# Performance work log

Measured on AMD Instinct MI355X. Metric: run time of the kernel, lower is better.

Reference implementation:

```python
import math
import jax, jax.numpy as jnp
import numpy as np

B, L, S, H, E, D = 2, 2048, 2048, 8, 64, 64


def setup_inputs() -> dict:
    key = jax.random.key(0)
    kq, kk, kv = jax.random.split(key, 3)
    return {
        "queries": jax.random.normal(kq, (B, L, H, E), dtype=jnp.float32),
        "keys": jax.random.normal(kk, (B, S, H, E), dtype=jnp.float32),
        "values": jax.random.normal(kv, (B, S, H, D), dtype=jnp.float32),
    }


def reference(queries, keys, values):
    b, l, h, e = queries.shape
    s = keys.shape[1]
    # source truncates queries if L > S
    if l > s:
        queries = queries[:, :s]
        l = s
    # dense scores [B,H,L,S]
    scores = jnp.einsum('blhe,bshe->bhls', queries, keys)
    # sparsity measure per query: max - mean over keys
    M_sp = scores.max(axis=-1) - scores.sum(axis=-1) / s  # [B,H,L]
    # k = min(max(L*log(S),1), L); for S>=3 this equals L (all queries, reordered)
    k = min(int(max(l * math.log(s), 1)), l)
    _, top_k = jax.lax.top_k(M_sp, k)  # [B,H,k], descending by M_sp
    # gather selected query rows of the score matrix
    topk_scores = jnp.take_along_axis(scores, top_k[..., None], axis=2)  # [B,H,k,S]
    topk_scores = topk_scores - topk_scores.max(axis=-1, keepdims=True)
    A = jax.nn.softmax(topk_scores / math.sqrt(e), axis=-1)  # [B,H,k,S]
    # attend (output in top-k-permuted query order, as in source)
    V = jnp.einsum('bhls,bshd->blhd', A, values)  # [B,k,H,D]
    return V
```

## Files before the change

### kernel.cpp

```cpp
#include <hip/hip_runtime.h>
#include <math.h>

#define BB 2
#define LL 2048
#define SS 2048
#define HH 8
#define EE 64
#define DD 64
#define HE (HH * EE)


typedef __attribute__((ext_vector_type(8))) short   bf16x8;
typedef __attribute__((ext_vector_type(4))) float   f32x4;
typedef __attribute__((ext_vector_type(8))) unsigned short u16x8;
typedef __attribute__((ext_vector_type(4))) unsigned short u16x4;

__device__ __forceinline__ unsigned short f2bf(float x) {
    unsigned int u = __float_as_uint(x);
    return (unsigned short)((u + 0x7FFFu + ((u >> 16) & 1u)) >> 16);
}

__device__ __forceinline__ float rdlane(float v, int lane) {
    return __uint_as_float(
        (unsigned)__builtin_amdgcn_readlane((int)__float_as_uint(v), lane));
}

__global__ __launch_bounds__(256, 2)
void msp_blas(const float* __restrict__ Q, const float* __restrict__ K,
              float* __restrict__ m32, float* __restrict__ maxs) {
#pragma clang fp contract(off)
    const int bid = blockIdx.x;
    const int lt = bid & 31, bh = bid >> 5;
    const int h = bh & 7, b = bh >> 3;
    const int t = threadIdx.x, lq = t & 63, w = t >> 6;
    const int l = lt * 64 + lq;

    float qf[64];
    const float4* qrow = (const float4*)(Q + (((size_t)b * LL + l) * HH + h) * EE);
#pragma unroll
    for (int i = 0; i < 16; i++) {
        float4 v = qrow[i];
        qf[4*i] = v.x; qf[4*i+1] = v.y; qf[4*i+2] = v.z; qf[4*i+3] = v.w;
    }

    const float* Kw = K + (((size_t)b * SS) * HH + h) * EE + (size_t)w * 512 * HE;
    const float* gld = Kw + (size_t)(lq >> 4) * HE + (lq & 15) * 4;

    float4 A0 = *(const float4*)(gld);
    float4 B0 = *(const float4*)(gld + 4 * HE);

    float mx = -1e30f;
    float blk[4];
#pragma unroll 1
    for (int lf = 0; lf < 4; ++lf) {
        float r[8];
#pragma unroll 1
        for (int i8 = 0; i8 < 16; ++i8) {
            const int kc = lf * 128 + i8 * 8;
            const int kn = (kc < 504) ? kc + 8 : 504;

            float4 A1 = *(const float4*)(gld + (size_t)kn * HE);
            float4 B1 = *(const float4*)(gld + (size_t)(kn + 4) * HE);

            float c[8];
#pragma unroll
            for (int j = 0; j < 8; ++j) c[j] = 0.f;
#pragma unroll
            for (int j = 0; j < 4; ++j) {
#pragma unroll
                for (int e4 = 0; e4 < 16; ++e4) {
                    const int ln = j * 16 + e4;
                    c[j] = fmaf(qf[4*e4+0], rdlane(A0.x, ln), c[j]);
                    c[j] = fmaf(qf[4*e4+1], rdlane(A0.y, ln), c[j]);
                    c[j] = fmaf(qf[4*e4+2], rdlane(A0.z, ln), c[j]);
                    c[j] = fmaf(qf[4*e4+3], rdlane(A0.w, ln), c[j]);
                }
            }
#pragma unroll
            for (int j = 0; j < 4; ++j) {
#pragma unroll
                for (int e4 = 0; e4 < 16; ++e4) {
                    const int ln = j * 16 + e4;
                    c[4+j] = fmaf(qf[4*e4+0], rdlane(B0.x, ln), c[4+j]);
                    c[4+j] = fmaf(qf[4*e4+1], rdlane(B0.y, ln), c[4+j]);
                    c[4+j] = fmaf(qf[4*e4+2], rdlane(B0.z, ln), c[4+j]);
                    c[4+j] = fmaf(qf[4*e4+3], rdlane(B0.w, ln), c[4+j]);
                }
            }
#pragma unroll
            for (int j = 0; j < 8; ++j) {
                mx = fmaxf(mx, c[j]);
                if (i8 == 0) r[j] = c[j];
                else         r[j] = __fadd_rn(r[j], c[j]);
            }
            A0 = A1; B0 = B1;
        }
        blk[lf] = __fadd_rn(
            __fadd_rn(__fadd_rn(r[0], r[1]), __fadd_rn(r[2], r[3])),
            __fadd_rn(__fadd_rn(r[4], r[5]), __fadd_rn(r[6], r[7])));
    }
    const float sub = __fadd_rn(__fadd_rn(blk[0], blk[1]),
                                __fadd_rn(blk[2], blk[3]));

    __shared__ float smx[4][64], ssub[4][64];
    smx[w][lq] = mx; ssub[w][lq] = sub;
    __syncthreads();
    if (w == 0) {
        const float m_all = fmaxf(fmaxf(smx[0][lq], smx[1][lq]),
                                  fmaxf(smx[2][lq], smx[3][lq]));
        const float s2048 = __fadd_rn(__fadd_rn(ssub[0][lq], ssub[1][lq]),
                                      __fadd_rn(ssub[2][lq], ssub[3][lq]));
        const float mean = __fmul_rn(s2048, 0.00048828125f);
        m32[((size_t)bh << 11) + l]  = __fsub_rn(m_all, mean);
        maxs[((size_t)bh << 11) + l] = m_all;
    }
}

__global__ __launch_bounds__(256)
void sort_rank(const float* __restrict__ m32, int* __restrict__ rank) {
    __shared__ unsigned int k1[2048];
    __shared__ int pay[2048];
    const int bh = blockIdx.x;
    const int t = threadIdx.x;
    for (int i = t; i < 2048; i += 256) {
        unsigned int u = __float_as_uint(m32[((size_t)bh << 11) + i]);
        u = (u & 0x80000000u) ? ~u : (u | 0x80000000u);
        k1[i] = u; pay[i] = i;
    }
    __syncthreads();
    for (int k = 2; k <= 2048; k <<= 1) {
        for (int j = k >> 1; j > 0; j >>= 1) {
            for (int i = t; i < 2048; i += 256) {
                const int ixj = i ^ j;
                if (ixj > i) {
                    unsigned int a1 = k1[i], c1 = k1[ixj];
                    int pa = pay[i], pc = pay[ixj];
                    const bool pre = (a1 > c1) || (a1 == c1 && pa < pc);
                    const bool dir = ((i & k) == 0);
                    if (dir != pre) {
                        k1[i] = c1; k1[ixj] = a1;
                        pay[i] = pc; pay[ixj] = pa;
                    }
                }
            }
            __syncthreads();
        }
    }
    for (int i = t; i < 2048; i += 256)
        rank[((size_t)bh << 11) + pay[i]] = i;
}

__global__ __launch_bounds__(256, 2)
void flash_mfma(const float* __restrict__ Q, const float* __restrict__ K,
                const float* __restrict__ V, const float* __restrict__ maxs,
                const int* __restrict__ rank, float* __restrict__ out) {
    __shared__ unsigned short ldsK[64 * 72];
    __shared__ unsigned short ldsVT[64 * 72];
    __shared__ unsigned short ldsP[4 * 16 * 72];

    const int bid = blockIdx.x;
    const int bh = bid & 15, lt = bid >> 4;
    const int h = bh & 7, b = bh >> 3;
    const int t = threadIdx.x, lane = t & 63, w = t >> 6;
    const int quad = lane >> 4, cl = lane & 15;

    const size_t kvbase = (((size_t)b * SS) * HH + h) * EE;

    bf16x8 qa[2];
    {
        const float* qp = Q + (((size_t)b * LL + (lt * 64 + w * 16 + cl)) * HH + h) * EE
                          + quad * 8;
#pragma unroll
        for (int ef = 0; ef < 2; ++ef) {
            float4 a0 = *(const float4*)(qp + ef * 32);
            float4 a1 = *(const float4*)(qp + ef * 32 + 4);
            short* s = (short*)&qa[ef];
            s[0] = (short)f2bf(a0.x); s[1] = (short)f2bf(a0.y);
            s[2] = (short)f2bf(a0.z); s[3] = (short)f2bf(a0.w);
            s[4] = (short)f2bf(a1.x); s[5] = (short)f2bf(a1.y);
            s[6] = (short)f2bf(a1.z); s[7] = (short)f2bf(a1.w);
        }
    }

    float negpm[4];
    int rk[4];
#pragma unroll
    for (int reg = 0; reg < 4; ++reg) {
        const int qg = lt * 64 + w * 16 + quad * 4 + reg;
        negpm[reg] = -0.125f * maxs[((size_t)bh << 11) + qg];
        rk[reg]    = rank[((size_t)bh << 11) + qg];
    }

    f32x4 accO[4];
#pragma unroll
    for (int nt = 0; nt < 4; ++nt) accO[nt] = (f32x4){0.f, 0.f, 0.f, 0.f};
    float ell[4] = {0.f, 0.f, 0.f, 0.f};

    const int pbase = w * (16 * 72);

#pragma unroll 1
    for (int c0 = 0; c0 < SS; c0 += 64) {
        __syncthreads();
        {
            const int row = t >> 2, col0 = (t & 3) * 16;
            const float* gp = K + kvbase + (size_t)(c0 + row) * HE + col0;
            float4 f0 = ((const float4*)gp)[0];
            float4 f1 = ((const float4*)gp)[1];
            float4 f2 = ((const float4*)gp)[2];
            float4 f3 = ((const float4*)gp)[3];
            u16x8 w0 = { f2bf(f0.x), f2bf(f0.y), f2bf(f0.z), f2bf(f0.w),
                         f2bf(f1.x), f2bf(f1.y), f2bf(f1.z), f2bf(f1.w) };
            u16x8 w1 = { f2bf(f2.x), f2bf(f2.y), f2bf(f2.z), f2bf(f2.w),
                         f2bf(f3.x), f2bf(f3.y), f2bf(f3.z), f2bf(f3.w) };
            *(u16x8*)&ldsK[row * 72 + col0]     = w0;
            *(u16x8*)&ldsK[row * 72 + col0 + 8] = w1;
        }
        {
            const int s0 = (t & 15) * 4, d0 = (t >> 4) * 4;
            const float* gv = V + kvbase + (size_t)(c0 + s0) * HE + d0;
            float4 v0 = *(const float4*)(gv);
            float4 v1 = *(const float4*)(gv + HE);
            float4 v2 = *(const float4*)(gv + 2 * HE);
            float4 v3 = *(const float4*)(gv + 3 * HE);
            u16x4 p0 = { f2bf(v0.x), f2bf(v1.x), f2bf(v2.x), f2bf(v3.x) };
            u16x4 p1 = { f2bf(v0.y), f2bf(v1.y), f2bf(v2.y), f2bf(v3.y) };
            u16x4 p2 = { f2bf(v0.z), f2bf(v1.z), f2bf(v2.z), f2bf(v3.z) };
            u16x4 p3 = { f2bf(v0.w), f2bf(v1.w), f2bf(v2.w), f2bf(v3.w) };
            *(u16x4*)&ldsVT[(d0 + 0) * 72 + s0] = p0;
            *(u16x4*)&ldsVT[(d0 + 1) * 72 + s0] = p1;
            *(u16x4*)&ldsVT[(d0 + 2) * 72 + s0] = p2;
            *(u16x4*)&ldsVT[(d0 + 3) * 72 + s0] = p3;
        }
        __syncthreads();

        f32x4 Sc[4];
#pragma unroll
        for (int nt = 0; nt < 4; ++nt) {
            bf16x8 bk0 = *(const bf16x8*)&ldsK[(nt * 16 + cl) * 72 + quad * 8];
            bf16x8 bk1 = *(const bf16x8*)&ldsK[(nt * 16 + cl) * 72 + quad * 8 + 32];
            f32x4 z = (f32x4){0.f, 0.f, 0.f, 0.f};
            z = __builtin_amdgcn_mfma_f32_16x16x32_bf16(qa[0], bk0, z, 0, 0, 0);
            z = __builtin_amdgcn_mfma_f32_16x16x32_bf16(qa[1], bk1, z, 0, 0, 0);
            Sc[nt] = z;
        }

#pragma unroll
        for (int nt = 0; nt < 4; ++nt) {
#pragma unroll
            for (int reg = 0; reg < 4; ++reg) {
                const float p = __expf(fmaf(Sc[nt][reg], 0.125f, negpm[reg]));
                ell[reg] += p;
                ldsP[pbase + (quad * 4 + reg) * 72 + nt * 16 + cl] = f2bf(p);
            }
        }

        bf16x8 pa0 = *(const bf16x8*)&ldsP[pbase + cl * 72 + quad * 8];
        bf16x8 pa1 = *(const bf16x8*)&ldsP[pbase + cl * 72 + quad * 8 + 32];
#pragma unroll
        for (int nt = 0; nt < 4; ++nt) {
            bf16x8 bv0 = *(const bf16x8*)&ldsVT[(nt * 16 + cl) * 72 + quad * 8];
            bf16x8 bv1 = *(const bf16x8*)&ldsVT[(nt * 16 + cl) * 72 + quad * 8 + 32];
            accO[nt] = __builtin_amdgcn_mfma_f32_16x16x32_bf16(pa0, bv0, accO[nt], 0, 0, 0);
            accO[nt] = __builtin_amdgcn_mfma_f32_16x16x32_bf16(pa1, bv1, accO[nt], 0, 0, 0);
        }
    }

#pragma unroll
    for (int reg = 0; reg < 4; ++reg) {
        float e = ell[reg];
        e += __shfl_xor(e, 1);
        e += __shfl_xor(e, 2);
        e += __shfl_xor(e, 4);
        e += __shfl_xor(e, 8);
        ell[reg] = 1.0f / e;
    }

#pragma unroll
    for (int reg = 0; reg < 4; ++reg) {
        float* orow = out + (((size_t)b * LL + rk[reg]) * HH + h) * DD;
#pragma unroll
        for (int nt = 0; nt < 4; ++nt)
            orow[nt * 16 + cl] = accO[nt][reg] * ell[reg];
    }
}

extern "C" void kernel_launch(void* const* d_in, const int* in_sizes, int n_in,
                              void* d_out, int out_size, void* d_ws, size_t ws_size,
                              hipStream_t stream) {
    const float* Q = (const float*)d_in[0];
    const float* K = (const float*)d_in[1];
    const float* V = (const float*)d_in[2];
    float* out = (float*)d_out;

    float* m32  = (float*)d_ws;
    int*   rank = (int*)((char*)d_ws + 131072);
    float* maxs = (float*)((char*)d_ws + 262144);

    msp_blas<<<BB * HH * (LL / 64), 256, 0, stream>>>(Q, K, m32, maxs);
    sort_rank<<<BB * HH, 256, 0, stream>>>(m32, rank);
    flash_mfma<<<BB * HH * (LL / 64), 256, 0, stream>>>(Q, K, V, maxs, rank, out);
}
```

Before: 400.9 us.

## Double-buffer K/V tiles in LDS with register prefetch of next tile

Splits the K and V^T shared-memory tiles into two buffers. The next tile's global loads are issued before the current tile's MFMA work and written to the other buffer afterward, which removes one barrier per iteration and is meant to hide global load latency behind compute. The cost is twice the LDS for K/V and more live registers holding the prefetched float4s, which could lower occupancy under the launch bounds of two blocks per SM.

```diff
diff --git a/kernel.cpp b/kernel.cpp
--- a/kernel.cpp
+++ b/kernel.cpp
@@ -154,8 +154,8 @@
 void flash_mfma(const float* __restrict__ Q, const float* __restrict__ K,
                 const float* __restrict__ V, const float* __restrict__ maxs,
                 const int* __restrict__ rank, float* __restrict__ out) {
-    __shared__ unsigned short ldsK[64 * 72];
-    __shared__ unsigned short ldsVT[64 * 72];
+    __shared__ unsigned short ldsK[2][64 * 72];
+    __shared__ unsigned short ldsVT[2][64 * 72];
     __shared__ unsigned short ldsP[4 * 16 * 72];
 
     const int bid = blockIdx.x;
@@ -198,71 +198,104 @@
 
     const int pbase = w * (16 * 72);
 
+    const int krow = t >> 2, kcol = (t & 3) * 16;
+    const int vs0 = (t & 15) * 4, vd0 = (t >> 4) * 4;
+
+    {
+        const float* gp = K + kvbase + (size_t)krow * HE + kcol;
+        float4 f0 = ((const float4*)gp)[0];
+        float4 f1 = ((const float4*)gp)[1];
+        float4 f2 = ((const float4*)gp)[2];
+        float4 f3 = ((const float4*)gp)[3];
+        const float* gv = V + kvbase + (size_t)vs0 * HE + vd0;
+        float4 v0 = *(const float4*)(gv);
+        float4 v1 = *(const float4*)(gv + HE);
+        float4 v2 = *(const float4*)(gv + 2 * HE);
+        float4 v3 = *(const float4*)(gv + 3 * HE);
+        u16x8 w0 = { f2bf(f0.x), f2bf(f0.y), f2bf(f0.z), f2bf(f0.w),
+                     f2bf(f1.x), f2bf(f1.y), f2bf(f1.z), f2bf(f1.w) };
+        u16x8 w1 = { f2bf(f2.x), f2bf(f2.y), f2bf(f2.z), f2bf(f2.w),
+                     f2bf(f3.x), f2bf(f3.y), f2bf(f3.z), f2bf(f3.w) };
+        *(u16x8*)&ldsK[0][krow * 72 + kcol]     = w0;
+        *(u16x8*)&ldsK[0][krow * 72 + kcol + 8] = w1;
+        u16x4 p0 = { f2bf(v0.x), f2bf(v1.x), f2bf(v2.x), f2bf(v3.x) };
+        u16x4 p1 = { f2bf(v0.y), f2bf(v1.y), f2bf(v2.y), f2bf(v3.y) };
+        u16x4 p2 = { f2bf(v0.z), f2bf(v1.z), f2bf(v2.z), f2bf(v3.z) };
+        u16x4 p3 = { f2bf(v0.w), f2bf(v1.w), f2bf(v2.w), f2bf(v3.w) };
+        *(u16x4*)&ldsVT[0][(vd0 + 0) * 72 + vs0] = p0;
+        *(u16x4*)&ldsVT[0][(vd0 + 1) * 72 + vs0] = p1;
+        *(u16x4*)&ldsVT[0][(vd0 + 2) * 72 + vs0] = p2;
+        *(u16x4*)&ldsVT[0][(vd0 + 3) * 72 + vs0] = p3;
+    }
+    __syncthreads();
+
+    int cur = 0;
 #pragma unroll 1
     for (int c0 = 0; c0 < SS; c0 += 64) {
-        __syncthreads();
-        {
-            const int row = t >> 2, col0 = (t & 3) * 16;
-            const float* gp = K + kvbase + (size_t)(c0 + row) * HE + col0;
-            float4 f0 = ((const float4*)gp)[0];
-            float4 f1 = ((const float4*)gp)[1];
-            float4 f2 = ((const float4*)gp)[2];
-            float4 f3 = ((const float4*)gp)[3];
+        const bool more = (c0 + 64 < SS);
+        float4 f0, f1, f2, f3, v0, v1, v2, v3;
+        if (more) {
+            const float* gp = K + kvbase + (size_t)(c0 + 64 + krow) * HE + kcol;
+            f0 = ((const float4*)gp)[0];
+            f1 = ((const float4*)gp)[1];
+            f2 = ((const float4*)gp)[2];
+            f3 = ((const float4*)gp)[3];
+            const float* gv = V + kvbase + (size_t)(c0 + 64 + vs0) * HE + vd0;
+            v0 = *(const float4*)(gv);
+            v1 = *(const float4*)(gv + HE);
+            v2 = *(const float4*)(gv + 2 * HE);
+            v3 = *(const float4*)(gv + 3 * HE);
+        }
+
+        f32x4 Sc[4];
+#pragma unroll
+        for (int nt = 0; nt < 4; ++nt) {
+            bf16x8 bk0 = *(const bf16x8*)&ldsK[cur][(nt * 16 + cl) * 72 + quad * 8];
+            bf16x8 bk1 = *(const bf16x8*)&ldsK[cur][(nt * 16 + cl) * 72 + quad * 8 + 32];
+            f32x4 z = (f32x4){0.f, 0.f, 0.f, 0.f};
+            z = __builtin_amdgcn_mfma_f32_16x16x32_bf16(qa[0], bk0, z, 0, 0, 0);
+            z = __builtin_amdgcn_mfma_f32_16x16x32_bf16(qa[1], bk1, z, 0, 0, 0);
+            Sc[nt] = z;
+        }
+
+#pragma unroll
+        for (int nt = 0; nt < 4; ++nt) {
+#pragma unroll
+            for (int reg = 0; reg < 4; ++reg) {
+                const float p = __expf(fmaf(Sc[nt][reg], 0.125f, negpm[reg]));
+                ell[reg] += p;
+                ldsP[pbase + (quad * 4 + reg) * 72 + nt * 16 + cl] = f2bf(p);
+            }
+        }
+
+        bf16x8 pa0 = *(const bf16x8*)&ldsP[pbase + cl * 72 + quad * 8];
+        bf16x8 pa1 = *(const bf16x8*)&ldsP[pbase + cl * 72 + quad * 8 + 32];
+#pragma unroll
+        for (int nt = 0; nt < 4; ++nt) {
+            bf16x8 bv0 = *(const bf16x8*)&ldsVT[cur][(nt * 16 + cl) * 72 + quad * 8];
+            bf16x8 bv1 = *(const bf16x8*)&ldsVT[cur][(nt * 16 + cl) * 72 + quad * 8 + 32];
+            accO[nt] = __builtin_amdgcn_mfma_f32_16x16x32_bf16(pa0, bv0, accO[nt], 0, 0, 0);
+            accO[nt] = __builtin_amdgcn_mfma_f32_16x16x32_bf16(pa1, bv1, accO[nt], 0, 0, 0);
+        }
+
+        if (more) {
             u16x8 w0 = { f2bf(f0.x), f2bf(f0.y), f2bf(f0.z), f2bf(f0.w),
                          f2bf(f1.x), f2bf(f1.y), f2bf(f1.z), f2bf(f1.w) };
             u16x8 w1 = { f2bf(f2.x), f2bf(f2.y), f2bf(f2.z), f2bf(f2.w),
                          f2bf(f3.x), f2bf(f3.y), f2bf(f3.z), f2bf(f3.w) };
-            *(u16x8*)&ldsK[row * 72 + col0]     = w0;
-            *(u16x8*)&ldsK[row * 72 + col0 + 8] = w1;
-        }
-        {
-            const int s0 = (t & 15) * 4, d0 = (t >> 4) * 4;
-            const float* gv = V + kvbase + (size_t)(c0 + s0) * HE + d0;
-            float4 v0 = *(const float4*)(gv);
-            float4 v1 = *(const float4*)(gv + HE);
-            float4 v2 = *(const float4*)(gv + 2 * HE);
-            float4 v3 = *(const float4*)(gv + 3 * HE);
+            *(u16x8*)&ldsK[cur ^ 1][krow * 72 + kcol]     = w0;
+            *(u16x8*)&ldsK[cur ^ 1][krow * 72 + kcol + 8] = w1;
             u16x4 p0 = { f2bf(v0.x), f2bf(v1.x), f2bf(v2.x), f2bf(v3.x) };
             u16x4 p1 = { f2bf(v0.y), f2bf(v1.y), f2bf(v2.y), f2bf(v3.y) };
             u16x4 p2 = { f2bf(v0.z), f2bf(v1.z), f2bf(v2.z), f2bf(v3.z) };
             u16x4 p3 = { f2bf(v0.w), f2bf(v1.w), f2bf(v2.w), f2bf(v3.w) };
-            *(u16x4*)&ldsVT[(d0 + 0) * 72 + s0] = p0;
-            *(u16x4*)&ldsVT[(d0 + 1) * 72 + s0] = p1;
-            *(u16x4*)&ldsVT[(d0 + 2) * 72 + s0] = p2;
-            *(u16x4*)&ldsVT[(d0 + 3) * 72 + s0] = p3;
+            *(u16x4*)&ldsVT[cur ^ 1][(vd0 + 0) * 72 + vs0] = p0;
+            *(u16x4*)&ldsVT[cur ^ 1][(vd0 + 1) * 72 + vs0] = p1;
+            *(u16x4*)&ldsVT[cur ^ 1][(vd0 + 2) * 72 + vs0] = p2;
+            *(u16x4*)&ldsVT[cur ^ 1][(vd0 + 3) * 72 + vs0] = p3;
         }
         __syncthreads();
-
-        f32x4 Sc[4];
-#pragma unroll
-        for (int nt = 0; nt < 4; ++nt) {
-            bf16x8 bk0 = *(const bf16x8*)&ldsK[(nt * 16 + cl) * 72 + quad * 8];
-            bf16x8 bk1 = *(const bf16x8*)&ldsK[(nt * 16 + cl) * 72 + quad * 8 + 32];
-            f32x4 z = (f32x4){0.f, 0.f, 0.f, 0.f};
-            z = __builtin_amdgcn_mfma_f32_16x16x32_bf16(qa[0], bk0, z, 0, 0, 0);
-            z = __builtin_amdgcn_mfma_f32_16x16x32_bf16(qa[1], bk1, z, 0, 0, 0);
-            Sc[nt] = z;
-        }
-
-#pragma unroll
-        for (int nt = 0; nt < 4; ++nt) {
-#pragma unroll
-            for (int reg = 0; reg < 4; ++reg) {
-                const float p = __expf(fmaf(Sc[nt][reg], 0.125f, negpm[reg]));
-                ell[reg] += p;
-                ldsP[pbase + (quad * 4 + reg) * 72 + nt * 16 + cl] = f2bf(p);
-            }
-        }
-
-        bf16x8 pa0 = *(const bf16x8*)&ldsP[pbase + cl * 72 + quad * 8];
-        bf16x8 pa1 = *(const bf16x8*)&ldsP[pbase + cl * 72 + quad * 8 + 32];
-#pragma unroll
-        for (int nt = 0; nt < 4; ++nt) {
-            bf16x8 bv0 = *(const bf16x8*)&ldsVT[(nt * 16 + cl) * 72 + quad * 8];
-            bf16x8 bv1 = *(const bf16x8*)&ldsVT[(nt * 16 + cl) * 72 + quad * 8 + 32];
-            accO[nt] = __builtin_amdgcn_mfma_f32_16x16x32_bf16(pa0, bv0, accO[nt], 0, 0, 0);
-            accO[nt] = __builtin_amdgcn_mfma_f32_16x16x32_bf16(pa1, bv1, accO[nt], 0, 0, 0);
-        }
+        cur ^= 1;
     }
 
 #pragma unroll
```

Measured after the change: 401.3 us. Within noise of the previous version (+0.1%).
